# Performance work log

Hardware: AMD Instinct MI355X
Metric: run time of the kernel (lower is better)

## Reference

```python
import jax, jax.numpy as jnp
import numpy as np

B, C, IMG, P = 64, 3, 224, 16
S = P // 2
G = IMG // P                      # 14 patches per side
NP = G * G                        # 196
N = NP + 1                        # +cls token
DIM, DEPTH, H, DH = 384, 12, 12, 32
INNER = H * DH                    # 384
MLP, NCLS = 1536, 1000
PD = 7 * P * P                    # patch_dim = 1792
EPS = 1e-5


def layernorm(x, g, b):
    mu = x.mean(-1, keepdims=True)
    var = ((x - mu) ** 2).mean(-1, keepdims=True)
    return (x - mu) * jax.lax.rsqrt(var + EPS) * g + b


def setup_inputs() -> dict:
    key = jax.random.key(0)
    ks = jax.random.split(key, 24)
    nrm = lambda k, shp, sc: jax.random.normal(k, shp, jnp.float32) * sc
    d = {
        "img": nrm(ks[0], (B, C, IMG, IMG), 1.0),
        "patch_w": nrm(ks[1], (DIM, PD), 0.02),
        "patch_b": jnp.zeros((DIM,), jnp.float32),
        "pos_emb": nrm(ks[2], (1, N, DIM), 0.02),
        "cls_tok": nrm(ks[3], (1, 1, DIM), 0.02),
        "ln1_g": jnp.ones((DEPTH, DIM), jnp.float32),
        "ln1_b": jnp.zeros((DEPTH, DIM), jnp.float32),
        "qkv_w": nrm(ks[4], (DEPTH, 3 * INNER, DIM), 0.02),
        "scale": jax.random.uniform(ks[5], (DEPTH, H), jnp.float32),
        "out_w": nrm(ks[6], (DEPTH, DIM, INNER), 0.02),
        "out_b": jnp.zeros((DEPTH, DIM), jnp.float32),
        "ln2_g": jnp.ones((DEPTH, DIM), jnp.float32),
        "ln2_b": jnp.zeros((DEPTH, DIM), jnp.float32),
        "ff_w1": nrm(ks[7], (DEPTH, MLP, DIM), 0.02),
        "ff_b1": jnp.zeros((DEPTH, MLP), jnp.float32),
        "ff_w2": nrm(ks[8], (DEPTH, DIM, MLP), 0.02),
        "ff_b2": jnp.zeros((DEPTH, DIM), jnp.float32),
        "lnf_g": jnp.ones((DIM,), jnp.float32),
        "lnf_b": jnp.zeros((DIM,), jnp.float32),
        "head_w": nrm(ks[9], (NCLS, DIM), 0.02),
        "head_b": jnp.zeros((NCLS,), jnp.float32),
    }
    return d


def reference(img, patch_w, patch_b, pos_emb, cls_tok, ln1_g, ln1_b, qkv_w,
              scale, out_w, out_b, ln2_g, ln2_b, ff_w1, ff_b1, ff_w2, ff_b2,
              lnf_g, lnf_b, head_w, head_b):
    # --- PatchShifting: pad, channel-mean, 4 shifted crops, concat to 7ch ---
    xp = jnp.pad(img, ((0, 0), (0, 0), (S, S), (S, S)))
    m = xp.mean(axis=1, keepdims=True)                     # [B,1,H+2S,W+2S]
    x_l2 = m[:, :, S:-S, : -2 * S]
    x_r2 = m[:, :, S:-S, 2 * S:]
    x_t2 = m[:, :, : -2 * S, S:-S]
    x_b2 = m[:, :, 2 * S:, S:-S]
    xc = jnp.concatenate([img, x_l2, x_r2, x_t2, x_b2], axis=1)  # [B,7,IMG,IMG]
    # --- patchify: b c (h p1) (w p2) -> b (h w) (p1 p2 c) ---
    patches = xc.reshape(B, 7, G, P, G, P).transpose(0, 2, 4, 3, 5, 1).reshape(B, NP, PD)
    x = patches @ patch_w.T + patch_b                     # [B,NP,DIM]
    x = jnp.concatenate([jnp.broadcast_to(cls_tok, (B, 1, DIM)), x], axis=1)
    x = x + pos_emb
    eye = jnp.eye(N, dtype=bool)
    for i in range(DEPTH):
        h = layernorm(x, ln1_g[i], ln1_b[i])
        qkv = h @ qkv_w[i].T                               # [B,N,3*INNER]
        q, k, v = jnp.split(qkv, 3, axis=-1)
        q = q.reshape(B, N, H, DH).transpose(0, 2, 1, 3)
        k = k.reshape(B, N, H, DH).transpose(0, 2, 1, 3)
        v = v.reshape(B, N, H, DH).transpose(0, 2, 1, 3)
        dots = jnp.einsum("bhid,bhjd->bhij", q, k) * scale[i][None, :, None, None]
        dots = jnp.where(eye, -jnp.inf, dots)              # diagonal self-mask
        attn = jax.nn.softmax(dots, axis=-1)
        o = jnp.einsum("bhij,bhjd->bhid", attn, v)
        o = o.transpose(0, 2, 1, 3).reshape(B, N, INNER)
        x = o @ out_w[i].T + out_b[i] + x
        h2 = layernorm(x, ln2_g[i], ln2_b[i])
        ff = jax.nn.gelu(h2 @ ff_w1[i].T + ff_b1[i], approximate=False)
        x = ff @ ff_w2[i].T + ff_b2[i] + x
    cls = layernorm(x[:, 0], lnf_g, lnf_b)
    return cls @ head_w.T + head_b                         # [B, NCLS]
```

## Files before the change

kernel.cpp:

```cpp
#include <hip/hip_runtime.h>
#include <hip/hip_bf16.h>

#define B_ 64
#define IMG_ 224
#define P_ 16
#define G_ 14
#define NP_ 196
#define N_ 197
#define DIM_ 384
#define DEPTH_ 12
#define H_ 12
#define DH_ 32
#define INNER_ 384
#define MLP_ 1536
#define NCLS_ 1000
#define PD_ 1792
#define EPS_ 1e-5f

typedef __hip_bfloat16 bf16;
using bf16x8 = __attribute__((ext_vector_type(8))) short;
using f32x4  = __attribute__((ext_vector_type(4))) float;

typedef __attribute__((address_space(1))) const void gas_void;
typedef __attribute__((address_space(3))) void las_void;

__device__ __forceinline__ float b2f(bf16 x) { return __bfloat162float(x); }
__device__ __forceinline__ bf16 f2b(float x) { return __float2bfloat16(x); }
__device__ __forceinline__ short f2b_raw(float f) {
    unsigned x = __float_as_uint(f);
    unsigned r = (x + 0x7FFFu + ((x >> 16) & 1u)) >> 16;
    return (short)r;
}
__device__ __forceinline__ void barrier_raw() {
    asm volatile("s_barrier" ::: "memory");
}
__device__ __forceinline__ void waitcnt_vm8() {
    asm volatile("s_waitcnt vmcnt(8)" ::: "memory");
}
__device__ __forceinline__ void waitcnt_vm0() {
    asm volatile("s_waitcnt vmcnt(0)" ::: "memory");
}
__device__ __forceinline__ void lgkm0_fence() {
    asm volatile("s_waitcnt lgkmcnt(0)" ::: "memory");
    __builtin_amdgcn_sched_barrier(0);
}

__global__ __launch_bounds__(256) void wconv_kernel(const float* __restrict__ src,
                                                    bf16* __restrict__ dst, int n4) {
    int i = blockIdx.x * 256 + threadIdx.x;
    if (i >= n4) return;
    float4 v = ((const float4*)src)[i];
    short4 o;
    o.x = f2b_raw(v.x); o.y = f2b_raw(v.y);
    o.z = f2b_raw(v.z); o.w = f2b_raw(v.w);
    ((short4*)dst)[i] = o;
}

__global__ __launch_bounds__(256) void mean_kernel(const float* __restrict__ img,
                                                   bf16* __restrict__ meanimg) {
    int idx = blockIdx.x * 256 + threadIdx.x;
    if (idx >= B_ * 50176) return;
    int b = idx / 50176;
    int yx = idx - b * 50176;
    const float* p = img + (size_t)b * 3 * 50176 + yx;
    meanimg[idx] = f2b((p[0] + p[50176] + p[100352]) * (1.0f / 3.0f));
}

__global__ __launch_bounds__(256) void patches_kernel(const float* __restrict__ img,
                                                      const bf16* __restrict__ meanimg,
                                                      bf16* __restrict__ patches,
                                                      int bp0, int nbp) {
    int idx = blockIdx.x * 256 + threadIdx.x;
    if (idx >= nbp * 256) return;
    int pix = idx & 255;
    int px = pix & 15, py = pix >> 4;
    int lbp = idx >> 8;
    int bp = bp0 + lbp;
    int p = bp % NP_;
    int b = bp / NP_;
    int gy = p / G_, gx = p - gy * G_;
    int y = gy * P_ + py, x = gx * P_ + px;
    const float* ib = img + (size_t)b * 3 * 50176 + y * 224 + x;
    bf16* out = patches + (size_t)lbp * PD_ + pix * 7;
    out[0] = f2b(ib[0]);
    out[1] = f2b(ib[50176]);
    out[2] = f2b(ib[100352]);
    const bf16* mb = meanimg + (size_t)b * 50176;
    out[3] = (x >= 8)  ? mb[y * 224 + x - 8]   : f2b(0.0f);
    out[4] = (x < 216) ? mb[y * 224 + x + 8]   : f2b(0.0f);
    out[5] = (y >= 8)  ? mb[(y - 8) * 224 + x] : f2b(0.0f);
    out[6] = (y < 216) ? mb[(y + 8) * 224 + x] : f2b(0.0f);
}

__global__ __launch_bounds__(256) void addpos_kernel(const bf16* __restrict__ pe,
                                                     const float* __restrict__ cls_tok,
                                                     const float* __restrict__ pos_emb,
                                                     float* __restrict__ x) {
    int idx = blockIdx.x * 256 + threadIdx.x;
    if (idx >= B_ * N_ * DIM_) return;
    int c = idx % DIM_;
    int r = idx / DIM_;
    int t = r % N_;
    int b = r / N_;
    float v = (t == 0) ? cls_tok[c]
                       : b2f(pe[((size_t)(b * NP_ + t - 1)) * DIM_ + c]);
    x[idx] = v + pos_emb[t * DIM_ + c];
}

__global__ __launch_bounds__(256) void ln_kernel(const float* __restrict__ in,
                                                 long in_stride,
                                                 const float* __restrict__ g,
                                                 const float* __restrict__ bb,
                                                 bf16* __restrict__ out, int rows) {
    int wave = threadIdx.x >> 6;
    int lane = threadIdx.x & 63;
    int row = blockIdx.x * 4 + wave;
    if (row >= rows) return;
    const float* p = in + (size_t)row * in_stride;
    float v[6];
    float s = 0.0f, s2 = 0.0f;
#pragma unroll
    for (int i = 0; i < 6; i++) {
        v[i] = p[lane + 64 * i];
        s += v[i];
        s2 += v[i] * v[i];
    }
#pragma unroll
    for (int m = 32; m >= 1; m >>= 1) {
        s += __shfl_xor(s, m);
        s2 += __shfl_xor(s2, m);
    }
    float mu = s * (1.0f / 384.0f);
    float var = s2 * (1.0f / 384.0f) - mu * mu;
    var = fmaxf(var, 0.0f);
    float inv = rsqrtf(var + EPS_);
    bf16* q = out + (size_t)row * DIM_;
#pragma unroll
    for (int i = 0; i < 6; i++) {
        int c = lane + 64 * i;
        q[c] = f2b((v[i] - mu) * inv * g[c] + bb[c]);
    }
}

__global__ __launch_bounds__(256) void head_kernel(const bf16* __restrict__ cls,
                                                   const float* __restrict__ W,
                                                   const float* __restrict__ bias,
                                                   float* __restrict__ out) {
    int wv = threadIdx.x >> 6, lane = threadIdx.x & 63;
    int col = blockIdx.x * 4 + wv;
    if (col >= NCLS_) return;
    const float* wp = W + (size_t)col * DIM_;
    float wreg[6];
#pragma unroll
    for (int i = 0; i < 6; i++) wreg[i] = wp[i * 64 + lane];
    float hb = bias[col];
    float res = 0.0f;
    for (int r = 0; r < 64; r++) {
        const bf16* ar = cls + r * DIM_;
        float s = 0.0f;
#pragma unroll
        for (int i = 0; i < 6; i++) s += b2f(ar[i * 64 + lane]) * wreg[i];
#pragma unroll
        for (int m = 32; m >= 1; m >>= 1) s += __shfl_xor(s, m);
        if (lane == r) res = s + hb;
    }
    out[(size_t)lane * NCLS_ + col] = res;
}

template <int MODE, typename OutT>
__global__ __launch_bounds__(256) void mgemm5_kernel(const bf16* __restrict__ A,
                                                     const bf16* __restrict__ W,
                                                     const float* __restrict__ bias,
                                                     const float* __restrict__ res,
                                                     OutT* __restrict__ C,
                                                     int M, int N, int K) {
    __shared__ __align__(16) short lds_a[2][128 * 64];
    __shared__ __align__(16) short lds_b[2][128 * 64];
    int tid = threadIdx.x;
    int wv = tid >> 6, lane = tid & 63;
    int ml = lane & 15, quad = lane >> 4;

    unsigned gx = gridDim.x;
    unsigned nwg = gx * gridDim.y;
    unsigned lid = blockIdx.y * gx + blockIdx.x;
    unsigned qc = nwg >> 3, rc = nwg & 7u;
    unsigned xcd = lid & 7u, loc = lid >> 3;
    unsigned nlid = (xcd < rc ? xcd * (qc + 1u)
                              : rc * (qc + 1u) + (xcd - rc) * qc) + loc;
    unsigned bx = nlid % gx, by = nlid / gx;
    int rowBase = by * 128, colBase = bx * 128;

    int l8 = lane >> 3;
    int c8 = lane & 7;
    int swsrc = ((c8 ^ l8) << 3);
    const bf16* aS[4];
    const bf16* bS[4];
#pragma unroll
    for (int j = 0; j < 4; j++) {
        int lr = wv * 32 + j * 8 + l8;
        int gr = rowBase + lr; if (gr >= M) gr = M - 1;
        aS[j] = A + (size_t)gr * K + swsrc;
        bS[j] = W + (size_t)(colBase + lr) * K + swsrc;
    }
    short* ldsA0 = &lds_a[0][0];
    short* ldsB0 = &lds_b[0][0];
    int dstOff = (wv * 32) * 64;

#define ISSUE_TILE5(bufi, t)                                                                        \
    do {                                                                                            \
        _Pragma("unroll")                                                                           \
        for (int j = 0; j < 4; j++) {                                                               \
            __builtin_amdgcn_global_load_lds((gas_void*)(aS[j] + (size_t)(t) * 64),                 \
                (las_void*)(ldsA0 + (bufi) * 8192 + dstOff + j * 512), 16, 0, 0);                   \
            __builtin_amdgcn_global_load_lds((gas_void*)(bS[j] + (size_t)(t) * 64),                 \
                (las_void*)(ldsB0 + (bufi) * 8192 + dstOff + j * 512), 16, 0, 0);                   \
        }                                                                                           \
    } while (0)

    int wr = (wv >> 1) * 64, wc = (wv & 1) * 64;
    int sw0 = ((quad ^ (ml & 7)) << 3);
    int sw1 = (((4 + quad) ^ (ml & 7)) << 3);
    f32x4 acc[4][4] = {};
    int NT = K >> 6;

    ISSUE_TILE5(0, 0);
    ISSUE_TILE5(1, 1);

    for (int t = 0; t < NT; t++) {
        if (t + 1 < NT) waitcnt_vm8();
        else            waitcnt_vm0();
        barrier_raw();
        int cb = t & 1;
        const short* pa = &lds_a[cb][0];
        const short* pb = &lds_b[cb][0];

        bf16x8 af0[4], bf0[4];
#pragma unroll
        for (int rg = 0; rg < 4; rg++)
            af0[rg] = *(const bf16x8*)(pa + (wr + rg * 16 + ml) * 64 + sw0);
#pragma unroll
        for (int cg = 0; cg < 4; cg++)
            bf0[cg] = *(const bf16x8*)(pb + (wc + cg * 16 + ml) * 64 + sw0);
        lgkm0_fence();
        __builtin_amdgcn_s_setprio(1);
#pragma unroll
        for (int rg = 0; rg < 4; rg++)
#pragma unroll
            for (int cg = 0; cg < 4; cg++)
                acc[rg][cg] = __builtin_amdgcn_mfma_f32_16x16x32_bf16(af0[rg], bf0[cg], acc[rg][cg], 0, 0, 0);
        __builtin_amdgcn_s_setprio(0);

        bf16x8 af1[4], bf1[4];
#pragma unroll
        for (int rg = 0; rg < 4; rg++)
            af1[rg] = *(const bf16x8*)(pa + (wr + rg * 16 + ml) * 64 + sw1);
#pragma unroll
        for (int cg = 0; cg < 4; cg++)
            bf1[cg] = *(const bf16x8*)(pb + (wc + cg * 16 + ml) * 64 + sw1);
        lgkm0_fence();
        __builtin_amdgcn_s_setprio(1);
#pragma unroll
        for (int rg = 0; rg < 4; rg++)
#pragma unroll
            for (int cg = 0; cg < 4; cg++)
                acc[rg][cg] = __builtin_amdgcn_mfma_f32_16x16x32_bf16(af1[rg], bf1[cg], acc[rg][cg], 0, 0, 0);
        __builtin_amdgcn_s_setprio(0);

        barrier_raw();
        if (t + 2 < NT) ISSUE_TILE5(cb, t + 2);
    }
#undef ISSUE_TILE5

    float bval[4];
#pragma unroll
    for (int cg = 0; cg < 4; cg++)
        bval[cg] = bias ? bias[colBase + wc + cg * 16 + ml] : 0.0f;

#pragma unroll
    for (int rg = 0; rg < 4; rg++) {
#pragma unroll
        for (int reg = 0; reg < 4; reg++) {
            int r = rowBase + wr + rg * 16 + quad * 4 + reg;
            if (r >= M) continue;
            size_t ro = (size_t)r * N;
#pragma unroll
            for (int cg = 0; cg < 4; cg++) {
                int c = colBase + wc + cg * 16 + ml;
                float v = acc[rg][cg][reg] + bval[cg];
                if constexpr (MODE == 1) v += res[ro + c];
                if constexpr (MODE == 2) v = 0.5f * v * (1.0f + erff(v * 0.70710678118f));
                C[ro + c] = (OutT)v;
            }
        }
    }
}

template <int MODE, typename OutT>
__global__ __launch_bounds__(256) void mgemm_kernel(const bf16* __restrict__ A,
                                                    const float* __restrict__ W,
                                                    const float* __restrict__ bias,
                                                    const float* __restrict__ res,
                                                    OutT* __restrict__ C,
                                                    int M, int N, int K) {
    __shared__ __align__(16) short lds_a[128 * 32];
    __shared__ __align__(16) short lds_b[64 * 32];
    int tid = threadIdx.x;
    int rowBase = blockIdx.y * 128;
    int colBase = blockIdx.x * 64;
    int w = tid >> 6, lane = tid & 63;
    int ml = lane & 15, kseg = lane >> 4;

    int ar = tid >> 1;
    int ah = (tid & 1) * 16;
    int agr = rowBase + ar;
    if (agr > M - 1) agr = M - 1;
    const float4* asrc_base = (const float4*)(A + (size_t)agr * K + ah);
    int br = tid >> 2;
    int bs = (tid & 3) * 8;
    const float4* wsrc_base = (const float4*)(W + (size_t)(colBase + br) * K + bs);

    f32x4 acc[2][4] = {};

    for (int k0 = 0; k0 < K; k0 += 32) {
        const float4* asrc = (const float4*)((const bf16*)asrc_base + k0);
        float4 av0 = asrc[0];
        float4 av1 = asrc[1];
        const float4* wsrc = (const float4*)((const float*)wsrc_base + k0);
        float4 w0 = wsrc[0];
        float4 w1 = wsrc[1];
        bf16x8 wb;
        wb[0] = f2b_raw(w0.x); wb[1] = f2b_raw(w0.y);
        wb[2] = f2b_raw(w0.z); wb[3] = f2b_raw(w0.w);
        wb[4] = f2b_raw(w1.x); wb[5] = f2b_raw(w1.y);
        wb[6] = f2b_raw(w1.z); wb[7] = f2b_raw(w1.w);
        __syncthreads();
        *(float4*)(lds_a + ar * 32 + ah) = av0;
        *(float4*)(lds_a + ar * 32 + ah + 8) = av1;
        *(bf16x8*)(lds_b + br * 32 + bs) = wb;
        __syncthreads();
        bf16x8 af0 = *(const bf16x8*)(lds_a + (w * 32 + ml) * 32 + kseg * 8);
        bf16x8 af1 = *(const bf16x8*)(lds_a + (w * 32 + 16 + ml) * 32 + kseg * 8);
#pragma unroll
        for (int ct = 0; ct < 4; ct++) {
            bf16x8 bf_ = *(const bf16x8*)(lds_b + (ct * 16 + ml) * 32 + kseg * 8);
            acc[0][ct] = __builtin_amdgcn_mfma_f32_16x16x32_bf16(af0, bf_, acc[0][ct], 0, 0, 0);
            acc[1][ct] = __builtin_amdgcn_mfma_f32_16x16x32_bf16(af1, bf_, acc[1][ct], 0, 0, 0);
        }
    }

    float bval[4];
#pragma unroll
    for (int ct = 0; ct < 4; ct++)
        bval[ct] = bias ? bias[colBase + ct * 16 + ml] : 0.0f;

#pragma unroll
    for (int rt = 0; rt < 2; rt++) {
#pragma unroll
        for (int reg = 0; reg < 4; reg++) {
            int r = rowBase + w * 32 + rt * 16 + kseg * 4 + reg;
            if (r >= M) continue;
            size_t ro = (size_t)r * N;
#pragma unroll
            for (int ct = 0; ct < 4; ct++) {
                int c = colBase + ct * 16 + ml;
                float v = acc[rt][ct][reg] + bval[ct];
                if constexpr (MODE == 1) v += res[ro + c];
                if constexpr (MODE == 2) v = 0.5f * v * (1.0f + erff(v * 0.70710678118f));
                C[ro + c] = (OutT)v;
            }
        }
    }
}

#define AKR 208
#define VTS 232
#define PSS 232
__global__ __launch_bounds__(256) void attn_mfma_kernel(const bf16* __restrict__ qkv,
                                                        const float* __restrict__ scale,
                                                        bf16* __restrict__ o) {
    __shared__ __align__(16) short Ks[AKR * 32];
    __shared__ __align__(16) short Vt[32 * VTS];
    __shared__ __align__(16) short Ps[4][16 * PSS];
    int b = blockIdx.x, h = blockIdx.y;
    int tid = threadIdx.x;
    int w = tid >> 6, lane = tid & 63;
    int ml = lane & 15, quad = lane >> 4;

    for (int i = tid; i < 32 * VTS / 2; i += 256) ((int*)Vt)[i] = 0;
    for (int e = lane; e < 16 * 16; e += 64) {
        int r = e >> 4, c = e & 15;
        Ps[w][r * PSS + 208 + c] = 0;
    }
    __syncthreads();
    for (int e = tid; e < AKR * 4; e += 256) {
        int row = e >> 2, seg = e & 3;
        float4 v = {0.0f, 0.0f, 0.0f, 0.0f};
        if (row < N_)
            v = *(const float4*)(qkv + (size_t)(b * N_ + row) * (3 * INNER_) + INNER_ + h * DH_ + seg * 8);
        *(float4*)(Ks + row * 32 + seg * 8) = v;
    }
    for (int e = tid; e < N_ * 32; e += 256) {
        int j = e >> 5, d = e & 31;
        Vt[d * VTS + j] = *(const short*)(qkv + (size_t)(b * N_ + j) * (3 * INNER_) + 2 * INNER_ + h * DH_ + d);
    }
    __syncthreads();

    float sc = scale[h];
    for (int qt = w; qt < 13; qt += 4) {
        int q0 = qt * 16;
        int qrow = q0 + ml;
        if (qrow > N_ - 1) qrow = N_ - 1;
        bf16x8 aq = *(const bf16x8*)(qkv + (size_t)(b * N_ + qrow) * (3 * INNER_) + h * DH_ + quad * 8);
        f32x4 accs[13];
#pragma unroll
        for (int kt = 0; kt < 13; kt++) {
            bf16x8 bk = *(const bf16x8*)(Ks + (kt * 16 + ml) * 32 + quad * 8);
            f32x4 z = {0.0f, 0.0f, 0.0f, 0.0f};
            accs[kt] = __builtin_amdgcn_mfma_f32_16x16x32_bf16(aq, bk, z, 0, 0, 0);
        }
        float rmax[4] = {-1e30f, -1e30f, -1e30f, -1e30f};
#pragma unroll
        for (int kt = 0; kt < 13; kt++) {
            int key = kt * 16 + ml;
#pragma unroll
            for (int reg = 0; reg < 4; reg++) {
                int qg = q0 + quad * 4 + reg;
                bool valid = (key < N_) && (key != qg);
                float s = valid ? accs[kt][reg] * sc : -1e30f;
                accs[kt][reg] = s;
                rmax[reg] = fmaxf(rmax[reg], s);
            }
        }
#pragma unroll
        for (int m = 1; m <= 8; m <<= 1)
#pragma unroll
            for (int reg = 0; reg < 4; reg++)
                rmax[reg] = fmaxf(rmax[reg], __shfl_xor(rmax[reg], m));
        float rsum[4] = {0.0f, 0.0f, 0.0f, 0.0f};
#pragma unroll
        for (int kt = 0; kt < 13; kt++) {
#pragma unroll
            for (int reg = 0; reg < 4; reg++) {
                float wgt = __expf(accs[kt][reg] - rmax[reg]);
                accs[kt][reg] = wgt;
                rsum[reg] += wgt;
            }
        }
#pragma unroll
        for (int m = 1; m <= 8; m <<= 1)
#pragma unroll
            for (int reg = 0; reg < 4; reg++)
                rsum[reg] += __shfl_xor(rsum[reg], m);
#pragma unroll
        for (int kt = 0; kt < 13; kt++)
#pragma unroll
            for (int reg = 0; reg < 4; reg++)
                Ps[w][(quad * 4 + reg) * PSS + kt * 16 + ml] = f2b_raw(accs[kt][reg]);
        f32x4 acco[2] = {{0.0f, 0.0f, 0.0f, 0.0f}, {0.0f, 0.0f, 0.0f, 0.0f}};
#pragma unroll
        for (int kc = 0; kc < 7; kc++) {
            bf16x8 ap = *(const bf16x8*)(Ps[w] + ml * PSS + kc * 32 + quad * 8);
#pragma unroll
            for (int nt = 0; nt < 2; nt++) {
                bf16x8 bv = *(const bf16x8*)(Vt + (nt * 16 + ml) * VTS + kc * 32 + quad * 8);
                acco[nt] = __builtin_amdgcn_mfma_f32_16x16x32_bf16(ap, bv, acco[nt], 0, 0, 0);
            }
        }
#pragma unroll
        for (int reg = 0; reg < 4; reg++) {
            int qg = q0 + quad * 4 + reg;
            if (qg >= N_) continue;
            float inv = 1.0f / rsum[reg];
#pragma unroll
            for (int nt = 0; nt < 2; nt++)
                o[(size_t)(b * N_ + qg) * INNER_ + h * DH_ + nt * 16 + ml] = f2b(acco[nt][reg] * inv);
        }
    }
}

__global__ __launch_bounds__(256) void diag_kernel(const float* __restrict__ bufx,
                                                   float* __restrict__ outf,
                                                   int base_marker, int ran) {
    __shared__ int bad;
    if (threadIdx.x == 0) bad = 0;
    __syncthreads();
    if (ran) {
        for (int i = threadIdx.x; i < 4096; i += 256) {
            float v = bufx[i];
            if (!(fabsf(v) < 1e30f)) bad = 1;
        }
    }
    __syncthreads();
    int marker = base_marker + (bad ? 512 : 0);
    if (marker == 0) return;
    int idx = blockIdx.x * 256 + threadIdx.x;
    if (idx > 0 && idx < 64000) outf[idx] = 0.0f;
    if (idx == 0) outf[0] = (float)marker;
}

extern "C" void kernel_launch(void* const* d_in, const int* in_sizes, int n_in,
                              void* d_out, int out_size, void* d_ws, size_t ws_size,
                              hipStream_t stream) {
    const float* img     = (const float*)d_in[0];
    const float* patch_w = (const float*)d_in[1];
    const float* patch_b = (const float*)d_in[2];
    const float* pos_emb = (const float*)d_in[3];
    const float* cls_tok = (const float*)d_in[4];
    const float* ln1_g   = (const float*)d_in[5];
    const float* ln1_b   = (const float*)d_in[6];
    const float* qkv_w   = (const float*)d_in[7];
    const float* scale   = (const float*)d_in[8];
    const float* out_w   = (const float*)d_in[9];
    const float* out_b   = (const float*)d_in[10];
    const float* ln2_g   = (const float*)d_in[11];
    const float* ln2_b   = (const float*)d_in[12];
    const float* ff_w1   = (const float*)d_in[13];
    const float* ff_b1   = (const float*)d_in[14];
    const float* ff_w2   = (const float*)d_in[15];
    const float* ff_b2   = (const float*)d_in[16];
    const float* lnf_g   = (const float*)d_in[17];
    const float* lnf_b   = (const float*)d_in[18];
    const float* head_w  = (const float*)d_in[19];
    const float* head_b  = (const float*)d_in[20];

    const size_t NEED      = 58146816;
    const size_t NEED_FAST = 101990400;
    const size_t NEED_FULL = 140722176;
    char* ws = (char*)d_ws;
    const int ROWS = B_ * N_;
    const int GY = (ROWS + 127) / 128;

    if (ws_size < NEED) {
        diag_kernel<<<250, 256, 0, stream>>>((const float*)d_out, (float*)d_out,
                                             1024 + (int)(ws_size >> 20), 0);
        return;
    }

    float* buf_x  = (float*)ws;
    bf16*  buf_hb = (bf16*)(ws + 19365888);

    if (ws_size >= NEED_FAST) {
        bool full = (ws_size >= NEED_FULL);
        bf16 *buf_qkv, *buf_ff, *buf_patch, *meanimg, *buf_cls;
        bf16 *wb_patch, *wb_qkv, *wb_out, *wb_ff1, *wb_ff2;
        int pchunks, fchunks;
        if (full) {
            buf_qkv  = (bf16*)(ws + 29048832);
            buf_ff   = (bf16*)(ws + 58097664);
            buf_patch= (bf16*)(ws + 29048832);
            meanimg  = (bf16*)(ws + 74006528);
            wb_patch = (bf16*)(ws + 96829440);
            wb_qkv   = (bf16*)(ws + 98205696);
            wb_out   = (bf16*)(ws + 108822528);
            wb_ff1   = (bf16*)(ws + 112361472);
            wb_ff2   = (bf16*)(ws + 126517248);
            buf_cls  = (bf16*)(ws + 140673024);
            pchunks = 1; fchunks = 1;
        } else {
            buf_qkv  = (bf16*)(ws + 29048832);
            buf_ff   = (bf16*)(ws + 29048832);
            buf_patch= (bf16*)(ws + 29048832);
            meanimg  = (bf16*)(ws + 29048832 + 22478848);
            buf_cls  = (bf16*)(ws + 58097664);
            wb_patch = (bf16*)(ws + 58146816);
            wb_qkv   = (bf16*)(ws + 59523072);
            wb_out   = (bf16*)(ws + 70139904);
            wb_ff1   = (bf16*)(ws + 73678848);
            wb_ff2   = (bf16*)(ws + 87834624);
            pchunks = 2; fchunks = 2;
        }

        wconv_kernel<<<(688128 / 4 + 255) / 256, 256, 0, stream>>>(patch_w, wb_patch, 688128 / 4);
        wconv_kernel<<<(5308416 / 4 + 255) / 256, 256, 0, stream>>>(qkv_w, wb_qkv, 5308416 / 4);
        wconv_kernel<<<(1769472 / 4 + 255) / 256, 256, 0, stream>>>(out_w, wb_out, 1769472 / 4);
        wconv_kernel<<<(7077888 / 4 + 255) / 256, 256, 0, stream>>>(ff_w1, wb_ff1, 7077888 / 4);
        wconv_kernel<<<(7077888 / 4 + 255) / 256, 256, 0, stream>>>(ff_w2, wb_ff2, 7077888 / 4);

        mean_kernel<<<(B_ * 50176 + 255) / 256, 256, 0, stream>>>(img, meanimg);
        for (int c = 0; c < pchunks; c++) {
            int bp0 = c * (12544 / pchunks);
            int nbp = 12544 / pchunks;
            patches_kernel<<<nbp, 256, 0, stream>>>(img, meanimg, buf_patch, bp0, nbp);
            mgemm5_kernel<0, bf16><<<dim3(3, (nbp + 127) / 128), 256, 0, stream>>>(
                buf_patch, wb_patch, patch_b, nullptr, buf_hb + (size_t)bp0 * DIM_, nbp, DIM_, PD_);
        }
        addpos_kernel<<<(B_ * N_ * DIM_ + 255) / 256, 256, 0, stream>>>(buf_hb, cls_tok, pos_emb, buf_x);

        for (int i = 0; i < DEPTH_; i++) {
            ln_kernel<<<ROWS / 4, 256, 0, stream>>>(buf_x, DIM_, ln1_g + i * DIM_,
                                                    ln1_b + i * DIM_, buf_hb, ROWS);
            mgemm5_kernel<0, bf16><<<dim3(9, GY), 256, 0, stream>>>(
                buf_hb, wb_qkv + (size_t)i * 3 * INNER_ * DIM_, nullptr, nullptr, buf_qkv,
                ROWS, 3 * INNER_, DIM_);
            attn_mfma_kernel<<<dim3(B_, H_), 256, 0, stream>>>(buf_qkv, scale + i * H_, buf_hb);
            mgemm5_kernel<1, float><<<dim3(3, GY), 256, 0, stream>>>(
                buf_hb, wb_out + (size_t)i * DIM_ * INNER_, out_b + i * DIM_, buf_x, buf_x,
                ROWS, DIM_, INNER_);
            ln_kernel<<<ROWS / 4, 256, 0, stream>>>(buf_x, DIM_, ln2_g + i * DIM_,
                                                    ln2_b + i * DIM_, buf_hb, ROWS);
            int base = 0;
            for (int c = 0; c < fchunks; c++) {
                int mrows = (fchunks == 1) ? ROWS : ((c == 0) ? 6336 : 6272);
                int gy = (mrows + 127) / 128;
                mgemm5_kernel<2, bf16><<<dim3(12, gy), 256, 0, stream>>>(
                    buf_hb + (size_t)base * DIM_, wb_ff1 + (size_t)i * MLP_ * DIM_,
                    ff_b1 + i * MLP_, nullptr, buf_ff, mrows, MLP_, DIM_);
                mgemm5_kernel<1, float><<<dim3(3, gy), 256, 0, stream>>>(
                    buf_ff, wb_ff2 + (size_t)i * DIM_ * MLP_, ff_b2 + i * DIM_,
                    buf_x + (size_t)base * DIM_, buf_x + (size_t)base * DIM_, mrows, DIM_, MLP_);
                base += mrows;
            }
        }

        ln_kernel<<<B_ / 4, 256, 0, stream>>>(buf_x, (long)N_ * DIM_, lnf_g, lnf_b, buf_cls, B_);
        head_kernel<<<250, 256, 0, stream>>>(buf_cls, head_w, head_b, (float*)d_out);
        diag_kernel<<<250, 256, 0, stream>>>(buf_x, (float*)d_out, 0, 1);
        return;
    }

    bf16* buf_cd   = (bf16*)(ws + 29048832);
    bf16* meanimg  = (bf16*)(ws + 29048832 + 22478848);
    bf16* buf_cls  = (bf16*)(ws + 58097664);

    mean_kernel<<<(B_ * 50176 + 255) / 256, 256, 0, stream>>>(img, meanimg);
    for (int c = 0; c < 2; c++) {
        int bp0 = c * 6272;
        patches_kernel<<<6272, 256, 0, stream>>>(img, meanimg, buf_cd, bp0, 6272);
        mgemm_kernel<0, bf16><<<dim3(DIM_ / 64, 49), 256, 0, stream>>>(
            buf_cd, patch_w, patch_b, nullptr, buf_hb + (size_t)bp0 * DIM_, 6272, DIM_, PD_);
    }
    addpos_kernel<<<(B_ * N_ * DIM_ + 255) / 256, 256, 0, stream>>>(buf_hb, cls_tok, pos_emb, buf_x);

    for (int i = 0; i < DEPTH_; i++) {
        ln_kernel<<<ROWS / 4, 256, 0, stream>>>(buf_x, DIM_, ln1_g + i * DIM_,
                                                ln1_b + i * DIM_, buf_hb, ROWS);
        mgemm_kernel<0, bf16><<<dim3((3 * INNER_) / 64, GY), 256, 0, stream>>>(
            buf_hb, qkv_w + (size_t)i * 3 * INNER_ * DIM_, nullptr, nullptr, buf_cd,
            ROWS, 3 * INNER_, DIM_);
        attn_mfma_kernel<<<dim3(B_, H_), 256, 0, stream>>>(buf_cd, scale + i * H_, buf_hb);
        mgemm_kernel<1, float><<<dim3(DIM_ / 64, GY), 256, 0, stream>>>(
            buf_hb, out_w + (size_t)i * DIM_ * INNER_, out_b + i * DIM_, buf_x, buf_x,
            ROWS, DIM_, INNER_);
        ln_kernel<<<ROWS / 4, 256, 0, stream>>>(buf_x, DIM_, ln2_g + i * DIM_,
                                                ln2_b + i * DIM_, buf_hb, ROWS);
        int base = 0;
        for (int c = 0; c < 2; c++) {
            int mrows = (c == 0) ? 6336 : 6272;
            int gy = (mrows + 127) / 128;
            mgemm_kernel<2, bf16><<<dim3(MLP_ / 64, gy), 256, 0, stream>>>(
                buf_hb + (size_t)base * DIM_, ff_w1 + (size_t)i * MLP_ * DIM_,
                ff_b1 + i * MLP_, nullptr, buf_cd, mrows, MLP_, DIM_);
            mgemm_kernel<1, float><<<dim3(DIM_ / 64, gy), 256, 0, stream>>>(
                buf_cd, ff_w2 + (size_t)i * DIM_ * MLP_, ff_b2 + i * DIM_,
                buf_x + (size_t)base * DIM_, buf_x + (size_t)base * DIM_, mrows, DIM_, MLP_);
            base += mrows;
        }
    }

    ln_kernel<<<B_ / 4, 256, 0, stream>>>(buf_x, (long)N_ * DIM_, lnf_g, lnf_b, buf_cls, B_);
    head_kernel<<<250, 256, 0, stream>>>(buf_cls, head_w, head_b, (float*)d_out);
    diag_kernel<<<250, 256, 0, stream>>>(buf_x, (float*)d_out, 0, 1);
}
```

Before: 2.223 ms.

## Add 256x128-tile double-buffered GEMM with XCD-aware block remap for QKV and FF1

Adds a new 512-thread GEMM kernel with 256x128 output tiles. It stages A and W through double-buffered LDS using direct global-to-LDS loads, and waits on vmcnt(3) so the next K-slice load overlaps the MFMA work. Block IDs are remapped so consecutive tiles land on the same XCD, which should improve L2 reuse. QKV and FF1 projections switch to it to cut per-tile load overhead; the larger tiles give fewer workgroups and more padding waste on the last row tile.

```diff
diff --git a/kernel.cpp b/kernel.cpp
--- a/kernel.cpp
+++ b/kernel.cpp
@@ -36,6 +36,9 @@
 }
 __device__ __forceinline__ void waitcnt_vm8() {
     asm volatile("s_waitcnt vmcnt(8)" ::: "memory");
+}
+__device__ __forceinline__ void waitcnt_vm3() {
+    asm volatile("s_waitcnt vmcnt(3)" ::: "memory");
 }
 __device__ __forceinline__ void waitcnt_vm0() {
     asm volatile("s_waitcnt vmcnt(0)" ::: "memory");
@@ -296,6 +299,105 @@
 }
 
 template <int MODE, typename OutT>
+__global__ __launch_bounds__(512) void mgemm9_kernel(const bf16* __restrict__ A,
+                                                     const bf16* __restrict__ W,
+                                                     const float* __restrict__ bias,
+                                                     const float* __restrict__ res,
+                                                     OutT* __restrict__ C,
+                                                     int M, int N, int K) {
+    __shared__ __align__(16) short lds_a[2][256 * 32];
+    __shared__ __align__(16) short lds_b[2][128 * 32];
+    int tid = threadIdx.x;
+    int wv = tid >> 6, lane = tid & 63;
+    int ml = lane & 15, quad = lane >> 4;
+
+    unsigned gx = gridDim.x;
+    unsigned nwg = gx * gridDim.y;
+    unsigned lid = blockIdx.y * gx + blockIdx.x;
+    unsigned qc = nwg >> 3, rc = nwg & 7u;
+    unsigned xcd = lid & 7u, loc = lid >> 3;
+    unsigned nlid = (xcd < rc ? xcd * (qc + 1u)
+                              : rc * (qc + 1u) + (xcd - rc) * qc) + loc;
+    unsigned bx = nlid % gx, by = nlid / gx;
+    int rowBase = by * 256, colBase = bx * 128;
+
+    int raA0 = tid >> 2,        caA0 = (tid & 3) * 8;
+    int raA1 = (tid + 512) >> 2, caA1 = (tid & 3) * 8;
+    int raB  = tid >> 2,        caB  = (tid & 3) * 8;
+    int gA0 = rowBase + raA0; if (gA0 >= M) gA0 = M - 1;
+    int gA1 = rowBase + raA1; if (gA1 >= M) gA1 = M - 1;
+    const bf16* aS0 = A + (size_t)gA0 * K + caA0;
+    const bf16* aS1 = A + (size_t)gA1 * K + caA1;
+    const bf16* bS  = W + (size_t)(colBase + raB) * K + caB;
+    short* ldsA0 = &lds_a[0][0];
+    short* ldsB0 = &lds_b[0][0];
+    int dA0 = tid * 8;
+    int dA1 = 4096 + tid * 8;
+    int dB  = tid * 8;
+
+#define ISSUE9(bufi, k0)                                                                              \
+    do {                                                                                              \
+        __builtin_amdgcn_global_load_lds((gas_void*)(aS0 + (k0)), (las_void*)(ldsA0 + (bufi) * 8192 + dA0), 16, 0, 0); \
+        __builtin_amdgcn_global_load_lds((gas_void*)(aS1 + (k0)), (las_void*)(ldsA0 + (bufi) * 8192 + dA1), 16, 0, 0); \
+        __builtin_amdgcn_global_load_lds((gas_void*)(bS  + (k0)), (las_void*)(ldsB0 + (bufi) * 4096 + dB),  16, 0, 0); \
+    } while (0)
+
+    int wr = (wv >> 1) * 64, wc = (wv & 1) * 64;
+    f32x4 acc[4][4] = {};
+    int NK = K >> 5;
+
+    ISSUE9(0, 0);
+    ISSUE9(1, 32);
+
+    for (int k = 0; k < NK; k++) {
+        if (k + 1 < NK) waitcnt_vm3();
+        else            waitcnt_vm0();
+        barrier_raw();
+        int cb = k & 1;
+        const short* pa = &lds_a[cb][0];
+        const short* pb = &lds_b[cb][0];
+        bf16x8 af[4], bfr[4];
+#pragma unroll
+        for (int rg = 0; rg < 4; rg++)
+            af[rg] = *(const bf16x8*)(pa + (wr + rg * 16 + ml) * 32 + quad * 8);
+#pragma unroll
+        for (int cg = 0; cg < 4; cg++)
+            bfr[cg] = *(const bf16x8*)(pb + (wc + cg * 16 + ml) * 32 + quad * 8);
+#pragma unroll
+        for (int rg = 0; rg < 4; rg++)
+#pragma unroll
+            for (int cg = 0; cg < 4; cg++)
+                acc[rg][cg] = __builtin_amdgcn_mfma_f32_16x16x32_bf16(af[rg], bfr[cg], acc[rg][cg], 0, 0, 0);
+        barrier_raw();
+        if (k + 2 < NK) ISSUE9(cb, (k + 2) * 32);
+    }
+#undef ISSUE9
+
+    float bval[4];
+#pragma unroll
+    for (int cg = 0; cg < 4; cg++)
+        bval[cg] = bias ? bias[colBase + wc + cg * 16 + ml] : 0.0f;
+
+#pragma unroll
+    for (int rg = 0; rg < 4; rg++) {
+#pragma unroll
+        for (int reg = 0; reg < 4; reg++) {
+            int r = rowBase + wr + rg * 16 + quad * 4 + reg;
+            if (r >= M) continue;
+            size_t ro = (size_t)r * N;
+#pragma unroll
+            for (int cg = 0; cg < 4; cg++) {
+                int c = colBase + wc + cg * 16 + ml;
+                float v = acc[rg][cg][reg] + bval[cg];
+                if constexpr (MODE == 1) v += res[ro + c];
+                if constexpr (MODE == 2) v = 0.5f * v * (1.0f + erff(v * 0.70710678118f));
+                C[ro + c] = (OutT)v;
+            }
+        }
+    }
+}
+
+template <int MODE, typename OutT>
 __global__ __launch_bounds__(256) void mgemm_kernel(const bf16* __restrict__ A,
                                                     const float* __restrict__ W,
                                                     const float* __restrict__ bias,
@@ -459,11 +561,11 @@
         f32x4 acco[2] = {{0.0f, 0.0f, 0.0f, 0.0f}, {0.0f, 0.0f, 0.0f, 0.0f}};
 #pragma unroll
         for (int kc = 0; kc < 7; kc++) {
-            bf16x8 ap = *(const bf16x8*)(Ps[w] + ml * PSS + kc * 32 + quad * 8);
+            bf16x8 ap2 = *(const bf16x8*)(Ps[w] + ml * PSS + kc * 32 + quad * 8);
 #pragma unroll
             for (int nt = 0; nt < 2; nt++) {
                 bf16x8 bv = *(const bf16x8*)(Vt + (nt * 16 + ml) * VTS + kc * 32 + quad * 8);
-                acco[nt] = __builtin_amdgcn_mfma_f32_16x16x32_bf16(ap, bv, acco[nt], 0, 0, 0);
+                acco[nt] = __builtin_amdgcn_mfma_f32_16x16x32_bf16(ap2, bv, acco[nt], 0, 0, 0);
             }
         }
 #pragma unroll
@@ -529,6 +631,7 @@
     char* ws = (char*)d_ws;
     const int ROWS = B_ * N_;
     const int GY = (ROWS + 127) / 128;
+    const int GY2 = (ROWS + 255) / 256;
 
     if (ws_size < NEED) {
         diag_kernel<<<250, 256, 0, stream>>>((const float*)d_out, (float*)d_out,
@@ -589,7 +692,7 @@
         for (int i = 0; i < DEPTH_; i++) {
             ln_kernel<<<ROWS / 4, 256, 0, stream>>>(buf_x, DIM_, ln1_g + i * DIM_,
                                                     ln1_b + i * DIM_, buf_hb, ROWS);
-            mgemm5_kernel<0, bf16><<<dim3(9, GY), 256, 0, stream>>>(
+            mgemm9_kernel<0, bf16><<<dim3(9, GY2), 512, 0, stream>>>(
                 buf_hb, wb_qkv + (size_t)i * 3 * INNER_ * DIM_, nullptr, nullptr, buf_qkv,
                 ROWS, 3 * INNER_, DIM_);
             attn_mfma_kernel<<<dim3(B_, H_), 256, 0, stream>>>(buf_qkv, scale + i * H_, buf_hb);
@@ -601,8 +704,9 @@
             int base = 0;
             for (int c = 0; c < fchunks; c++) {
                 int mrows = (fchunks == 1) ? ROWS : ((c == 0) ? 6336 : 6272);
+                int gy2 = (mrows + 255) / 256;
                 int gy = (mrows + 127) / 128;
-                mgemm5_kernel<2, bf16><<<dim3(12, gy), 256, 0, stream>>>(
+                mgemm9_kernel<2, bf16><<<dim3(12, gy2), 512, 0, stream>>>(
                     buf_hb + (size_t)base * DIM_, wb_ff1 + (size_t)i * MLP_ * DIM_,
                     ff_b1 + i * MLP_, nullptr, buf_ff, mrows, MLP_, DIM_);
                 mgemm5_kernel<1, float><<<dim3(3, gy), 256, 0, stream>>>(
```

After: 2.132 ms. 4.1% less time.
